# Kernel optimization log

Hardware: AMD Instinct MI355X
Metric: run time of the kernel (lower is better)

## Reference

```python
import jax, jax.numpy as jnp
import numpy as np

R, S, D, V, K, B, L, U, I = 20000, 64, 128, 50000, 32, 2048, 20480, 100000, 100000


def setup_inputs() -> dict:
    key = jax.random.key(0)
    ks = jax.random.split(key, 16)
    # segment ids: equal-sized history per batch element (guaranteed non-empty)
    seg = (jnp.arange(L, dtype=jnp.int32) // (L // B)).astype(jnp.int32)
    return {
        "user": jax.random.randint(ks[0], (B,), 0, U, dtype=jnp.int32),
        "item": jax.random.randint(ks[1], (B,), 0, I, dtype=jnp.int32),
        "historical_review": jax.random.randint(ks[2], (R, S), 0, V, dtype=jnp.int32),
        "historical_review_positive": jax.random.normal(ks[3], (R, D), jnp.float32),
        "user_hist_idx": jax.random.randint(ks[4], (L,), 0, R, dtype=jnp.int32),
        "user_hist_seg": seg,
        "item_hist_idx": jax.random.randint(ks[5], (L,), 0, R, dtype=jnp.int32),
        "item_hist_seg": seg,
        "word_emb": jax.random.normal(ks[6], (V, D), jnp.float32) * 0.02,
        "M_w": jax.random.normal(ks[7], (D, D), jnp.float32) * (1.0 / np.sqrt(D)),
        "M_b": jnp.zeros((D,), jnp.float32),
        "W_w": jax.random.normal(ks[8], (D, K), jnp.float32) * (1.0 / np.sqrt(D)),
        "W_b": jnp.zeros((K,), jnp.float32),
        "T_w": jax.random.normal(ks[9], (K, D), jnp.float32) * (1.0 / np.sqrt(K)),
        "T_b": jnp.zeros((D,), jnp.float32),
        "user_emb": jax.random.normal(ks[10], (U, D), jnp.float32) * 0.02,
        "item_emb": jax.random.normal(ks[11], (I, D), jnp.float32) * 0.02,
        "avg_rating": jnp.full((1,), 3.5, jnp.float32),
    }


def _segment_mean(x, seg, num_segments):
    s = jax.ops.segment_sum(x, seg, num_segments=num_segments)
    c = jax.ops.segment_sum(jnp.ones(seg.shape, x.dtype), seg, num_segments=num_segments)
    return s / jnp.maximum(c, 1.0)[:, None]


def reference(user, item, historical_review, historical_review_positive,
              user_hist_idx, user_hist_seg, item_hist_idx, item_hist_seg,
              word_emb, M_w, M_b, W_w, W_b, T_w, T_b,
              user_emb, item_emb, avg_rating):
    # --- aspect extraction (ABAE-style) over R historical reviews ---
    e_w = word_emb[historical_review]                      # [R, S, D] gather
    y_s = historical_review_positive                       # [R, D] sentence embedding
    # dx = transform_M(e_w) @ y_s  -> attention logits over words
    dx = jnp.einsum('rsd,de,re->rs', e_w, M_w, y_s) + jnp.einsum('d,rd->r', M_b, y_s)[:, None]
    ax = jax.nn.softmax(dx, axis=1)                        # [R, S]
    z_s = jnp.einsum('rsd,rs->rd', e_w, ax)                # [R, D]
    p_t = jax.nn.softmax(z_s @ W_w + W_b, axis=1)          # [R, K] aspect probs
    r_s = p_t @ T_w + T_b                                  # [R, D] aspect-based review embedding
    # --- ragged gather + mean-pool over user/item histories ---
    ua = _segment_mean(r_s[user_hist_idx], user_hist_seg, B)  # [B, D]
    ia = _segment_mean(r_s[item_hist_idx], item_hist_seg, B)  # [B, D]
    uf = user_emb[user]                                    # [B, D]
    itf = item_emb[item]                                   # [B, D]
    prediction = jnp.sum(ua * ia, axis=-1) + jnp.sum(uf * itf, axis=-1) + avg_rating[0]
    return prediction  # [B]
```

## Files before the change

### kernel.cpp

```cpp
#include <hip/hip_runtime.h>


typedef __attribute__((ext_vector_type(8))) short bf16x8;
typedef __attribute__((ext_vector_type(4))) float f32x4;
typedef __attribute__((ext_vector_type(2))) float vf2;

__device__ __forceinline__ unsigned int f2bf_rne(float x) {
  unsigned int u = __float_as_uint(x);
  return (u + 0x7fffu + ((u >> 16) & 1u)) >> 16;
}

__global__ __launch_bounds__(256) void kA0_pack(
    const float* __restrict__ Mw, const float* __restrict__ Ww,
    uint4* __restrict__ Wpk) {
  int c = blockIdx.x * 256 + threadIdx.x;
  if (c >= 2560) return;
  int cl = c & 63, g = c >> 6;
  int jt = g >> 2, ks = g & 3;
  int n = jt * 16 + (cl & 15);
  int k0 = ks * 32 + (cl >> 4) * 8;
  float v[8];
#pragma unroll
  for (int j = 0; j < 8; ++j) {
    int e = k0 + j;
    v[j] = (n < 128) ? Mw[(size_t)e * 128 + n] : Ww[(size_t)e * 32 + (n - 128)];
  }
  uint4 pk;
  pk.x = f2bf_rne(v[0]) | (f2bf_rne(v[1]) << 16);
  pk.y = f2bf_rne(v[2]) | (f2bf_rne(v[3]) << 16);
  pk.z = f2bf_rne(v[4]) | (f2bf_rne(v[5]) << 16);
  pk.w = f2bf_rne(v[6]) | (f2bf_rne(v[7]) << 16);
  Wpk[c] = pk;
}

__global__ __launch_bounds__(256) void kA_mfma(
    const float* __restrict__ We, const uint4* __restrict__ Wpk,
    unsigned char* __restrict__ Z, unsigned char* __restrict__ WW8, int V) {
  __shared__ uint4 Bs[2560];
  int t = threadIdx.x;
  int L = t & 63, wid = t >> 6;

#pragma unroll
  for (int q = 0; q < 10; ++q) Bs[t + q * 256] = Wpk[t + q * 256];
  __syncthreads();

  int r0 = blockIdx.x * 64;
  if (r0 > V - 64) r0 = V - 64;
  int rowA = r0 + wid * 16 + (L & 15);
  const float4* Arow = (const float4*)(We + (size_t)rowA * 128);

  f32x4 acc[10];
#pragma unroll
  for (int jt = 0; jt < 10; ++jt) acc[jt] = (f32x4){0.f, 0.f, 0.f, 0.f};

#pragma unroll
  for (int ks = 0; ks < 4; ++ks) {
    int koff4 = ks * 8 + (L >> 4) * 2;
    float4 a0 = Arow[koff4];
    float4 a1 = Arow[koff4 + 1];
    union { uint4 u; bf16x8 v; } A;
    A.u.x = f2bf_rne(a0.x) | (f2bf_rne(a0.y) << 16);
    A.u.y = f2bf_rne(a0.z) | (f2bf_rne(a0.w) << 16);
    A.u.z = f2bf_rne(a1.x) | (f2bf_rne(a1.y) << 16);
    A.u.w = f2bf_rne(a1.z) | (f2bf_rne(a1.w) << 16);
#pragma unroll
    for (int jt = 0; jt < 10; ++jt) {
      union { uint4 u; bf16x8 v; } Bf;
      Bf.u = Bs[(jt * 4 + ks) * 64 + L];
      acc[jt] = __builtin_amdgcn_mfma_f32_16x16x32_bf16(A.v, Bf.v, acc[jt], 0, 0, 0);
    }
  }

#pragma unroll
  for (int jt = 0; jt < 10; ++jt) {
#pragma unroll
    for (int i = 0; i < 4; ++i) {
      float v0 = acc[jt][i] * 64.f;
      float v1 = __shfl_xor(v0, 1);
      float v2 = __shfl_xor(v0, 2);
      float v3 = __shfl_xor(v0, 3);
      if (!(L & 3)) {
        int col = jt * 16 + (L & 15);
        int orow = r0 + wid * 16 + (L >> 4) * 4 + i;
        int w8 = __builtin_amdgcn_cvt_pk_fp8_f32(v0, v1, 0, false);
        w8 = __builtin_amdgcn_cvt_pk_fp8_f32(v2, v3, w8, true);
        if (col < 128)
          *(int*)(Z + (size_t)orow * 128 + col) = w8;
        else
          *(int*)(WW8 + (size_t)orow * 32 + (col - 128)) = w8;
      }
    }
  }
}

__device__ __forceinline__ float dot_fp8_16(uint4 q, const float4* y) {
  float s = 0.f;
#pragma unroll
  for (int i = 0; i < 4; ++i) {
    unsigned int u = (&q.x)[i];
    vf2 a = __builtin_amdgcn_cvt_pk_f32_fp8(u, false);
    vf2 b = __builtin_amdgcn_cvt_pk_f32_fp8(u, true);
    float4 yv = y[i];
    s += a.x * yv.x + a.y * yv.y + b.x * yv.z + b.y * yv.w;
  }
  return s;
}

__global__ __launch_bounds__(256) void k3_review(
    const int* __restrict__ hr, const float* __restrict__ Y,
    const unsigned char* __restrict__ Z, const unsigned char* __restrict__ WW8,
    const float* __restrict__ Wb, const float* __restrict__ Tw,
    const float* __restrict__ Tb, float* __restrict__ rs, int R) {
  int t = threadIdx.x;
  int wv = t >> 6, lane = t & 63;
  int r = blockIdx.x * 4 + wv;
  if (r >= R) r = R - 1;

  int word = hr[(size_t)r * 64 + lane];
  int g = lane & 15, sub = lane >> 4;

  int wid_p[4];
#pragma unroll
  for (int p = 0; p < 4; ++p) wid_p[p] = __shfl(word, p * 16 + g);

  uint4 q0[4], q1[4];
  uint2 w8[4];
#pragma unroll
  for (int p = 0; p < 4; ++p) {
    const unsigned char* bp = Z + (size_t)wid_p[p] * 128;
    q0[p] = *(const uint4*)(bp + sub * 16);
    q1[p] = *(const uint4*)(bp + 64 + sub * 16);
    w8[p] = *(const uint2*)(WW8 + (size_t)wid_p[p] * 32 + sub * 8);
  }
  const float4* Yr = (const float4*)(Y + (size_t)r * 128);
  float4 ya[4], yb[4];
#pragma unroll
  for (int i = 0; i < 4; ++i) {
    ya[i] = Yr[sub * 4 + i];
    yb[i] = Yr[16 + sub * 4 + i];
  }

  float dxp[4];
#pragma unroll
  for (int p = 0; p < 4; ++p) {
    float acc = dot_fp8_16(q0[p], ya) + dot_fp8_16(q1[p], yb);
    acc += __shfl_xor(acc, 16);
    acc += __shfl_xor(acc, 32);
    dxp[p] = acc * 0.015625f;
  }
  float dx = dxp[0];
  dx = (sub == 1) ? dxp[1] : dx;
  dx = (sub == 2) ? dxp[2] : dx;
  dx = (sub == 3) ? dxp[3] : dx;

  float m = dx;
#pragma unroll
  for (int off = 32; off; off >>= 1) m = fmaxf(m, __shfl_xor(m, off));
  float ex = __expf(dx - m);
  float sum = ex;
#pragma unroll
  for (int off = 32; off; off >>= 1) sum += __shfl_xor(sum, off);
  float ax = ex / sum;

  float lacc[8];
#pragma unroll
  for (int j = 0; j < 8; ++j) lacc[j] = 0.f;
#pragma unroll
  for (int p = 0; p < 4; ++p) {
    float axp = __shfl(ax, p * 16 + g);
    vf2 a0 = __builtin_amdgcn_cvt_pk_f32_fp8(w8[p].x, false);
    vf2 a1 = __builtin_amdgcn_cvt_pk_f32_fp8(w8[p].x, true);
    vf2 a2 = __builtin_amdgcn_cvt_pk_f32_fp8(w8[p].y, false);
    vf2 a3 = __builtin_amdgcn_cvt_pk_f32_fp8(w8[p].y, true);
    lacc[0] += axp * a0.x; lacc[1] += axp * a0.y;
    lacc[2] += axp * a1.x; lacc[3] += axp * a1.y;
    lacc[4] += axp * a2.x; lacc[5] += axp * a2.y;
    lacc[6] += axp * a3.x; lacc[7] += axp * a3.y;
  }
#pragma unroll
  for (int off = 8; off; off >>= 1) {
#pragma unroll
    for (int j = 0; j < 8; ++j) lacc[j] += __shfl_xor(lacc[j], off);
  }
  const float4* Wb4 = (const float4*)Wb;
  float4 wba = Wb4[sub * 2], wbb = Wb4[sub * 2 + 1];
  lacc[0] = lacc[0] * 0.015625f + wba.x; lacc[1] = lacc[1] * 0.015625f + wba.y;
  lacc[2] = lacc[2] * 0.015625f + wba.z; lacc[3] = lacc[3] * 0.015625f + wba.w;
  lacc[4] = lacc[4] * 0.015625f + wbb.x; lacc[5] = lacc[5] * 0.015625f + wbb.y;
  lacc[6] = lacc[6] * 0.015625f + wbb.z; lacc[7] = lacc[7] * 0.015625f + wbb.w;

  float mk = lacc[0];
#pragma unroll
  for (int j = 1; j < 8; ++j) mk = fmaxf(mk, lacc[j]);
  mk = fmaxf(mk, __shfl_xor(mk, 16));
  mk = fmaxf(mk, __shfl_xor(mk, 32));
  float ek[8], sk = 0.f;
#pragma unroll
  for (int j = 0; j < 8; ++j) { ek[j] = __expf(lacc[j] - mk); sk += ek[j]; }
  sk += __shfl_xor(sk, 16);
  sk += __shfl_xor(sk, 32);
  float inv = 1.0f / sk;
  float pv[8];
#pragma unroll
  for (int j = 0; j < 8; ++j) pv[j] = ek[j] * inv;

  const float2* T2 = (const float2*)Tw;
  float2 acc2 = ((const float2*)Tb)[lane];
#pragma unroll
  for (int kk = 0; kk < 32; ++kk) {
    float pk = __shfl(pv[kk & 7], (kk >> 3) * 16);
    float2 tv = T2[kk * 64 + lane];
    acc2.x += pk * tv.x;
    acc2.y += pk * tv.y;
  }
  ((float2*)rs)[(size_t)r * 64 + lane] = acc2;
}

__global__ __launch_bounds__(256) void k4_final(
    const float* __restrict__ rs, const int* __restrict__ uidx,
    const int* __restrict__ iidx, const int* __restrict__ user,
    const int* __restrict__ item, const float* __restrict__ uemb,
    const float* __restrict__ iemb, const float* __restrict__ avg,
    float* __restrict__ out, int B, int per) {
  int t = threadIdx.x;
  int w = t >> 6, lane = t & 63;
  int b = blockIdx.x * 4 + w;
  if (b >= B) return;
  const float2* rs2 = (const float2*)rs;
  float2 ua = {0.f, 0.f}, ia = {0.f, 0.f};
  int base = b * per;
  for (int j = 0; j < per; ++j) {
    int id = uidx[base + j];
    float2 tv = rs2[(size_t)id * 64 + lane];
    ua.x += tv.x; ua.y += tv.y;
  }
  for (int j = 0; j < per; ++j) {
    int id = iidx[base + j];
    float2 tv = rs2[(size_t)id * 64 + lane];
    ia.x += tv.x; ia.y += tv.y;
  }
  float inv = 1.0f / (float)per;
  float part = (ua.x * ia.x + ua.y * ia.y) * inv * inv;
  float2 uf = ((const float2*)uemb)[(size_t)user[b] * 64 + lane];
  float2 itf = ((const float2*)iemb)[(size_t)item[b] * 64 + lane];
  part += uf.x * itf.x + uf.y * itf.y;
#pragma unroll
  for (int off = 32; off; off >>= 1) part += __shfl_xor(part, off);
  if (lane == 0) out[b] = part + avg[0];
}

extern "C" void kernel_launch(void* const* d_in, const int* in_sizes, int n_in,
                              void* d_out, int out_size, void* d_ws, size_t ws_size,
                              hipStream_t stream) {
  const int*   user = (const int*)d_in[0];
  const int*   item = (const int*)d_in[1];
  const int*   hr   = (const int*)d_in[2];
  const float* Y    = (const float*)d_in[3];
  const int*   uhi  = (const int*)d_in[4];
  const int*   ihi  = (const int*)d_in[6];
  const float* We   = (const float*)d_in[8];
  const float* Mw   = (const float*)d_in[9];
  const float* Ww   = (const float*)d_in[11];
  const float* Wb   = (const float*)d_in[12];
  const float* Tw   = (const float*)d_in[13];
  const float* Tb   = (const float*)d_in[14];
  const float* Ue   = (const float*)d_in[15];
  const float* Ie   = (const float*)d_in[16];
  const float* avg  = (const float*)d_in[17];

  int B = in_sizes[0];
  int R = in_sizes[3] / 128;
  int V = in_sizes[8] / 128;
  int L = in_sizes[4];
  int per = L / B;

  unsigned char* ws = (unsigned char*)d_ws;
  uint4* Wpk = (uint4*)ws;
  unsigned char* Z   = ws + 40960;
  unsigned char* WW8 = Z + (size_t)V * 128;
  float* rsbuf = (float*)(WW8 + (size_t)V * 32);
  float* out = (float*)d_out;

  kA0_pack<<<10, 256, 0, stream>>>(Mw, Ww, Wpk);
  kA_mfma<<<(V + 63) / 64, 256, 0, stream>>>(We, Wpk, Z, WW8, V);
  k3_review<<<(R + 3) / 4, 256, 0, stream>>>(hr, Y, Z, WW8, Wb, Tw, Tb, rsbuf, R);
  k4_final<<<(B + 3) / 4, 256, 0, stream>>>(rsbuf, uhi, ihi, user, item, Ue, Ie, avg, out, B, per);
}
```

Before: 237.8 us.

## Defer T projection past mean-pooling and process two reviews per wave

The review kernel now writes the 32-wide aspect probabilities p_t instead of the 128-wide r_s, and the final kernel averages p_t over each history before applying T_w and T_b once per batch element. This relies on linearity of the mean, cuts the per-review T matmul and reduces the gathered bytes per history entry by a factor of four. The review kernel also handles two reviews per wave to put more gather loads in flight, at the cost of higher register pressure.

```diff
diff --git a/kernel.cpp b/kernel.cpp
--- a/kernel.cpp
+++ b/kernel.cpp
@@ -109,138 +109,150 @@
 __global__ __launch_bounds__(256) void k3_review(
     const int* __restrict__ hr, const float* __restrict__ Y,
     const unsigned char* __restrict__ Z, const unsigned char* __restrict__ WW8,
-    const float* __restrict__ Wb, const float* __restrict__ Tw,
-    const float* __restrict__ Tb, float* __restrict__ rs, int R) {
+    const float* __restrict__ Wb, float* __restrict__ pOut, int R) {
   int t = threadIdx.x;
   int wv = t >> 6, lane = t & 63;
-  int r = blockIdx.x * 4 + wv;
-  if (r >= R) r = R - 1;
-
-  int word = hr[(size_t)r * 64 + lane];
   int g = lane & 15, sub = lane >> 4;
-
-  int wid_p[4];
-#pragma unroll
-  for (int p = 0; p < 4; ++p) wid_p[p] = __shfl(word, p * 16 + g);
-
-  uint4 q0[4], q1[4];
-  uint2 w8[4];
+  int rbase = (blockIdx.x * 4 + wv) * 2;
+  int r0 = rbase < R ? rbase : R - 1;
+  int r1 = rbase + 1 < R ? rbase + 1 : R - 1;
+
+  int word0 = hr[(size_t)r0 * 64 + lane];
+  int word1 = hr[(size_t)r1 * 64 + lane];
+
+  uint4 q0[2][4], q1[2][4];
+  uint2 w8[2][4];
 #pragma unroll
   for (int p = 0; p < 4; ++p) {
-    const unsigned char* bp = Z + (size_t)wid_p[p] * 128;
-    q0[p] = *(const uint4*)(bp + sub * 16);
-    q1[p] = *(const uint4*)(bp + 64 + sub * 16);
-    w8[p] = *(const uint2*)(WW8 + (size_t)wid_p[p] * 32 + sub * 8);
-  }
-  const float4* Yr = (const float4*)(Y + (size_t)r * 128);
-  float4 ya[4], yb[4];
-#pragma unroll
-  for (int i = 0; i < 4; ++i) {
-    ya[i] = Yr[sub * 4 + i];
-    yb[i] = Yr[16 + sub * 4 + i];
-  }
-
-  float dxp[4];
-#pragma unroll
-  for (int p = 0; p < 4; ++p) {
-    float acc = dot_fp8_16(q0[p], ya) + dot_fp8_16(q1[p], yb);
-    acc += __shfl_xor(acc, 16);
-    acc += __shfl_xor(acc, 32);
-    dxp[p] = acc * 0.015625f;
-  }
-  float dx = dxp[0];
-  dx = (sub == 1) ? dxp[1] : dx;
-  dx = (sub == 2) ? dxp[2] : dx;
-  dx = (sub == 3) ? dxp[3] : dx;
-
-  float m = dx;
-#pragma unroll
-  for (int off = 32; off; off >>= 1) m = fmaxf(m, __shfl_xor(m, off));
-  float ex = __expf(dx - m);
-  float sum = ex;
-#pragma unroll
-  for (int off = 32; off; off >>= 1) sum += __shfl_xor(sum, off);
-  float ax = ex / sum;
-
-  float lacc[8];
-#pragma unroll
-  for (int j = 0; j < 8; ++j) lacc[j] = 0.f;
-#pragma unroll
-  for (int p = 0; p < 4; ++p) {
-    float axp = __shfl(ax, p * 16 + g);
-    vf2 a0 = __builtin_amdgcn_cvt_pk_f32_fp8(w8[p].x, false);
-    vf2 a1 = __builtin_amdgcn_cvt_pk_f32_fp8(w8[p].x, true);
-    vf2 a2 = __builtin_amdgcn_cvt_pk_f32_fp8(w8[p].y, false);
-    vf2 a3 = __builtin_amdgcn_cvt_pk_f32_fp8(w8[p].y, true);
-    lacc[0] += axp * a0.x; lacc[1] += axp * a0.y;
-    lacc[2] += axp * a1.x; lacc[3] += axp * a1.y;
-    lacc[4] += axp * a2.x; lacc[5] += axp * a2.y;
-    lacc[6] += axp * a3.x; lacc[7] += axp * a3.y;
-  }
-#pragma unroll
-  for (int off = 8; off; off >>= 1) {
-#pragma unroll
-    for (int j = 0; j < 8; ++j) lacc[j] += __shfl_xor(lacc[j], off);
+    int wa = __shfl(word0, p * 16 + g);
+    int wb = __shfl(word1, p * 16 + g);
+    const unsigned char* ba = Z + (size_t)wa * 128;
+    const unsigned char* bb = Z + (size_t)wb * 128;
+    q0[0][p] = *(const uint4*)(ba + sub * 16);
+    q1[0][p] = *(const uint4*)(ba + 64 + sub * 16);
+    w8[0][p] = *(const uint2*)(WW8 + (size_t)wa * 32 + sub * 8);
+    q0[1][p] = *(const uint4*)(bb + sub * 16);
+    q1[1][p] = *(const uint4*)(bb + 64 + sub * 16);
+    w8[1][p] = *(const uint2*)(WW8 + (size_t)wb * 32 + sub * 8);
   }
   const float4* Wb4 = (const float4*)Wb;
   float4 wba = Wb4[sub * 2], wbb = Wb4[sub * 2 + 1];
-  lacc[0] = lacc[0] * 0.015625f + wba.x; lacc[1] = lacc[1] * 0.015625f + wba.y;
-  lacc[2] = lacc[2] * 0.015625f + wba.z; lacc[3] = lacc[3] * 0.015625f + wba.w;
-  lacc[4] = lacc[4] * 0.015625f + wbb.x; lacc[5] = lacc[5] * 0.015625f + wbb.y;
-  lacc[6] = lacc[6] * 0.015625f + wbb.z; lacc[7] = lacc[7] * 0.015625f + wbb.w;
-
-  float mk = lacc[0];
-#pragma unroll
-  for (int j = 1; j < 8; ++j) mk = fmaxf(mk, lacc[j]);
-  mk = fmaxf(mk, __shfl_xor(mk, 16));
-  mk = fmaxf(mk, __shfl_xor(mk, 32));
-  float ek[8], sk = 0.f;
-#pragma unroll
-  for (int j = 0; j < 8; ++j) { ek[j] = __expf(lacc[j] - mk); sk += ek[j]; }
-  sk += __shfl_xor(sk, 16);
-  sk += __shfl_xor(sk, 32);
-  float inv = 1.0f / sk;
-  float pv[8];
-#pragma unroll
-  for (int j = 0; j < 8; ++j) pv[j] = ek[j] * inv;
-
-  const float2* T2 = (const float2*)Tw;
-  float2 acc2 = ((const float2*)Tb)[lane];
-#pragma unroll
-  for (int kk = 0; kk < 32; ++kk) {
-    float pk = __shfl(pv[kk & 7], (kk >> 3) * 16);
-    float2 tv = T2[kk * 64 + lane];
-    acc2.x += pk * tv.x;
-    acc2.y += pk * tv.y;
-  }
-  ((float2*)rs)[(size_t)r * 64 + lane] = acc2;
+
+#pragma unroll
+  for (int v = 0; v < 2; ++v) {
+    int r = v ? r1 : r0;
+    const float4* Yr = (const float4*)(Y + (size_t)r * 128);
+    float4 ya[4], yb[4];
+#pragma unroll
+    for (int i = 0; i < 4; ++i) {
+      ya[i] = Yr[sub * 4 + i];
+      yb[i] = Yr[16 + sub * 4 + i];
+    }
+
+    float dxp[4];
+#pragma unroll
+    for (int p = 0; p < 4; ++p) {
+      float acc = dot_fp8_16(q0[v][p], ya) + dot_fp8_16(q1[v][p], yb);
+      acc += __shfl_xor(acc, 16);
+      acc += __shfl_xor(acc, 32);
+      dxp[p] = acc * 0.015625f;
+    }
+    float dx = dxp[0];
+    dx = (sub == 1) ? dxp[1] : dx;
+    dx = (sub == 2) ? dxp[2] : dx;
+    dx = (sub == 3) ? dxp[3] : dx;
+
+    float m = dx;
+#pragma unroll
+    for (int off = 32; off; off >>= 1) m = fmaxf(m, __shfl_xor(m, off));
+    float ex = __expf(dx - m);
+    float sum = ex;
+#pragma unroll
+    for (int off = 32; off; off >>= 1) sum += __shfl_xor(sum, off);
+    float ax = ex / sum;
+
+    float lacc[8];
+#pragma unroll
+    for (int j = 0; j < 8; ++j) lacc[j] = 0.f;
+#pragma unroll
+    for (int p = 0; p < 4; ++p) {
+      float axp = __shfl(ax, p * 16 + g);
+      vf2 a0 = __builtin_amdgcn_cvt_pk_f32_fp8(w8[v][p].x, false);
+      vf2 a1 = __builtin_amdgcn_cvt_pk_f32_fp8(w8[v][p].x, true);
+      vf2 a2 = __builtin_amdgcn_cvt_pk_f32_fp8(w8[v][p].y, false);
+      vf2 a3 = __builtin_amdgcn_cvt_pk_f32_fp8(w8[v][p].y, true);
+      lacc[0] += axp * a0.x; lacc[1] += axp * a0.y;
+      lacc[2] += axp * a1.x; lacc[3] += axp * a1.y;
+      lacc[4] += axp * a2.x; lacc[5] += axp * a2.y;
+      lacc[6] += axp * a3.x; lacc[7] += axp * a3.y;
+    }
+#pragma unroll
+    for (int off = 8; off; off >>= 1) {
+#pragma unroll
+      for (int j = 0; j < 8; ++j) lacc[j] += __shfl_xor(lacc[j], off);
+    }
+    lacc[0] = lacc[0] * 0.015625f + wba.x; lacc[1] = lacc[1] * 0.015625f + wba.y;
+    lacc[2] = lacc[2] * 0.015625f + wba.z; lacc[3] = lacc[3] * 0.015625f + wba.w;
+    lacc[4] = lacc[4] * 0.015625f + wbb.x; lacc[5] = lacc[5] * 0.015625f + wbb.y;
+    lacc[6] = lacc[6] * 0.015625f + wbb.z; lacc[7] = lacc[7] * 0.015625f + wbb.w;
+
+    float mk = lacc[0];
+#pragma unroll
+    for (int j = 1; j < 8; ++j) mk = fmaxf(mk, lacc[j]);
+    mk = fmaxf(mk, __shfl_xor(mk, 16));
+    mk = fmaxf(mk, __shfl_xor(mk, 32));
+    float ek[8], sk = 0.f;
+#pragma unroll
+    for (int j = 0; j < 8; ++j) { ek[j] = __expf(lacc[j] - mk); sk += ek[j]; }
+    sk += __shfl_xor(sk, 16);
+    sk += __shfl_xor(sk, 32);
+    float inv = 1.0f / sk;
+
+    if (g == 0) {
+      float4 o0, o1;
+      o0.x = ek[0] * inv; o0.y = ek[1] * inv; o0.z = ek[2] * inv; o0.w = ek[3] * inv;
+      o1.x = ek[4] * inv; o1.y = ek[5] * inv; o1.z = ek[6] * inv; o1.w = ek[7] * inv;
+      float* dst = pOut + (size_t)r * 32 + sub * 8;
+      *(float4*)dst = o0;
+      *(float4*)(dst + 4) = o1;
+    }
+  }
 }
 
 __global__ __launch_bounds__(256) void k4_final(
-    const float* __restrict__ rs, const int* __restrict__ uidx,
+    const float* __restrict__ p, const int* __restrict__ uidx,
     const int* __restrict__ iidx, const int* __restrict__ user,
     const int* __restrict__ item, const float* __restrict__ uemb,
-    const float* __restrict__ iemb, const float* __restrict__ avg,
+    const float* __restrict__ iemb, const float* __restrict__ Tw,
+    const float* __restrict__ Tb, const float* __restrict__ avg,
     float* __restrict__ out, int B, int per) {
   int t = threadIdx.x;
   int w = t >> 6, lane = t & 63;
   int b = blockIdx.x * 4 + w;
   if (b >= B) return;
-  const float2* rs2 = (const float2*)rs;
-  float2 ua = {0.f, 0.f}, ia = {0.f, 0.f};
+
+  int k = lane & 31;
+  const int* idx = (lane < 32) ? uidx : iidx;
+  float pbar = 0.f;
   int base = b * per;
   for (int j = 0; j < per; ++j) {
-    int id = uidx[base + j];
-    float2 tv = rs2[(size_t)id * 64 + lane];
-    ua.x += tv.x; ua.y += tv.y;
-  }
-  for (int j = 0; j < per; ++j) {
-    int id = iidx[base + j];
-    float2 tv = rs2[(size_t)id * 64 + lane];
-    ia.x += tv.x; ia.y += tv.y;
-  }
-  float inv = 1.0f / (float)per;
-  float part = (ua.x * ia.x + ua.y * ia.y) * inv * inv;
+    int id = idx[base + j];
+    pbar += p[(size_t)id * 32 + k];
+  }
+  pbar *= 1.0f / (float)per;
+
+  const float2* T2 = (const float2*)Tw;
+  float2 tb2 = ((const float2*)Tb)[lane];
+  float2 ua = tb2, ia = tb2;
+#pragma unroll 8
+  for (int kk = 0; kk < 32; ++kk) {
+    float pu = __shfl(pbar, kk);
+    float pi = __shfl(pbar, 32 + kk);
+    float2 tv = T2[kk * 64 + lane];
+    ua.x += pu * tv.x; ua.y += pu * tv.y;
+    ia.x += pi * tv.x; ia.y += pi * tv.y;
+  }
+  float part = ua.x * ia.x + ua.y * ia.y;
   float2 uf = ((const float2*)uemb)[(size_t)user[b] * 64 + lane];
   float2 itf = ((const float2*)iemb)[(size_t)item[b] * 64 + lane];
   part += uf.x * itf.x + uf.y * itf.y;
@@ -278,11 +290,12 @@
   uint4* Wpk = (uint4*)ws;
   unsigned char* Z   = ws + 40960;
   unsigned char* WW8 = Z + (size_t)V * 128;
-  float* rsbuf = (float*)(WW8 + (size_t)V * 32);
+  float* pbuf = (float*)(WW8 + (size_t)V * 32);
   float* out = (float*)d_out;
 
   kA0_pack<<<10, 256, 0, stream>>>(Mw, Ww, Wpk);
   kA_mfma<<<(V + 63) / 64, 256, 0, stream>>>(We, Wpk, Z, WW8, V);
-  k3_review<<<(R + 3) / 4, 256, 0, stream>>>(hr, Y, Z, WW8, Wb, Tw, Tb, rsbuf, R);
-  k4_final<<<(B + 3) / 4, 256, 0, stream>>>(rsbuf, uhi, ihi, user, item, Ue, Ie, avg, out, B, per);
-}
+  k3_review<<<(R + 7) / 8, 256, 0, stream>>>(hr, Y, Z, WW8, Wb, pbuf, R);
+  k4_final<<<(B + 3) / 4, 256, 0, stream>>>(pbuf, uhi, ihi, user, item, Ue, Ie,
+                                            Tw, Tb, avg, out, B, per);
+}
```

After: 223.6 us. 1.06x faster.
